# Kernel tuning notes

Measured on AMD Instinct MI355X. Metric: run time of the kernel, lower is better.

The kernel has to match this reference:

```python
import jax, jax.numpy as jnp
import numpy as np

N_NODES = 200000
N_EDGES = 800000
C1, E1 = 20000, 80000
C2, E2 = 2000, 8000
N_IN, N_HID, K_BLOCK = 24, 64, 6
N_OUT = 6
BN_EPS = 1e-5


def cheb_conv(x, edge_index, W, b, n):
    """PyG ChebConv with lambda_max=2: L_hat = -D^-1/2 A D^-1/2."""
    src, dst = edge_index[0], edge_index[1]
    K = W.shape[0]
    deg = jax.ops.segment_sum(jnp.ones(src.shape[0], x.dtype), dst, num_segments=n)
    dis = jnp.where(deg > 0, 1.0 / jnp.sqrt(jnp.maximum(deg, 1.0)), 0.0)
    norm = -(dis[src] * dis[dst])[:, None]  # [E,1]

    def prop(h):
        return jax.ops.segment_sum(h[src] * norm, dst, num_segments=n)

    Tx0 = x
    out = Tx0 @ W[0]
    if K > 1:
        Tx1 = prop(Tx0)
        out = out + Tx1 @ W[1]
        for k in range(2, K):
            Tx2 = 2.0 * prop(Tx1) - Tx0
            out = out + Tx2 @ W[k]
            Tx0, Tx1 = Tx1, Tx2
    return out + b


def batchnorm(h, g, bt):
    m = jnp.mean(h, axis=0)
    v = jnp.mean((h - m) ** 2, axis=0)  # biased var, as torch BN forward
    return (h - m) / jnp.sqrt(v + BN_EPS) * g + bt


def kipf_block(x, edge_index, W, b, g, bt, n):
    return jax.nn.relu(batchnorm(cheb_conv(x, edge_index, W, b, n), g, bt))


def segment_mean(x, seg, n_seg):
    s = jax.ops.segment_sum(x, seg, num_segments=n_seg)
    cnt = jax.ops.segment_sum(jnp.ones(x.shape[0], x.dtype), seg, num_segments=n_seg)
    return s / jnp.maximum(cnt, 1.0)[:, None]


def setup_inputs() -> dict:
    key = jax.random.key(0)
    ks = jax.random.split(key, 12)
    inp = {
        "x": jax.random.normal(ks[0], (N_NODES, N_IN), jnp.float32),
        "edge_index": jax.random.randint(ks[1], (2, N_EDGES), 0, N_NODES),
        "cluster1": jax.random.randint(ks[2], (N_NODES,), 0, C1),
        "cluster2": jax.random.randint(ks[3], (N_NODES,), 0, C2),
        "edge_index_c1": jax.random.randint(ks[4], (2, E1), 0, C1),
        "edge_index_c2": jax.random.randint(ks[5], (2, E2), 0, C2),
    }
    sc = 1.0 / np.sqrt(N_IN * K_BLOCK)
    for i, kk in zip((1, 2, 3), (ks[6], ks[7], ks[8])):
        inp[f"W{i}"] = jax.random.normal(kk, (K_BLOCK, N_IN, N_HID), jnp.float32) * sc
        inp[f"b{i}"] = jnp.zeros((N_HID,), jnp.float32)
        inp[f"g{i}"] = jnp.ones((N_HID,), jnp.float32)
        inp[f"bt{i}"] = jnp.zeros((N_HID,), jnp.float32)
    n_mix = 3 * N_HID + N_IN
    inp["Wm"] = jax.random.normal(ks[9], (1, n_mix, N_OUT), jnp.float32) / np.sqrt(n_mix)
    inp["bm"] = jnp.zeros((N_OUT,), jnp.float32)
    return inp


def reference(x, edge_index, cluster1, cluster2, edge_index_c1, edge_index_c2,
              W1, b1, g1, bt1, W2, b2, g2, bt2, W3, b3, g3, bt3, Wm, bm):
    # branch 1: full-resolution graph
    h1 = kipf_block(x, edge_index, W1, b1, g1, bt1, N_NODES)
    # branch 2: cluster1-pooled graph, then unpool
    xp1 = segment_mean(x, cluster1, C1)
    h2 = kipf_block(xp1, edge_index_c1, W2, b2, g2, bt2, C1)[cluster1]
    # branch 3: cluster2-pooled graph, then unpool
    xp2 = segment_mean(x, cluster2, C2)
    h3 = kipf_block(xp2, edge_index_c2, W3, b3, g3, bt3, C2)[cluster2]
    # skip concat with raw input, then mixing conv (K=1 -> identity Cheb term)
    mix = jnp.concatenate([h1, h2, h3, x], axis=1)
    return cheb_conv(mix, edge_index, Wm, bm, N_NODES)
```

## Files before the change

### kernel.cpp

```cpp
#include <hip/hip_runtime.h>
#include <algorithm>

#define FIN 24
#define NHID 64
#define NMIX 216
#define NOUT 6
#define BN_EPS 1e-5f

__global__ void k_hist(const int* __restrict__ ei, int E, int* deg) {
    int e = blockIdx.x * blockDim.x + threadIdx.x;
    if (e < E) atomicAdd(&deg[ei[E + e]], 1);
}

__global__ void k_scan_local(const int* __restrict__ deg, int n, int* rowptr, int* bsum,
                             float* __restrict__ dis) {
    __shared__ int s[256];
    int i = blockIdx.x * 256 + threadIdx.x;
    int v = (i < n) ? deg[i] : 0;
    if (i < n) dis[i] = v > 0 ? rsqrtf((float)v) : 0.f;
    s[threadIdx.x] = v;
    __syncthreads();
#pragma unroll
    for (int off = 1; off < 256; off <<= 1) {
        int x = (threadIdx.x >= off) ? s[threadIdx.x - off] : 0;
        __syncthreads();
        s[threadIdx.x] += x;
        __syncthreads();
    }
    if (i <= n) rowptr[i] = s[threadIdx.x] - v;
    if (threadIdx.x == 255) bsum[blockIdx.x] = s[255];
}

__global__ void k_scan_bsum(int* bsum, int nb) {
    __shared__ int s[256];
    int carry = 0;
    for (int base = 0; base < nb; base += 256) {
        int i = base + threadIdx.x;
        int v = (i < nb) ? bsum[i] : 0;
        s[threadIdx.x] = v;
        __syncthreads();
#pragma unroll
        for (int off = 1; off < 256; off <<= 1) {
            int x = (threadIdx.x >= off) ? s[threadIdx.x - off] : 0;
            __syncthreads();
            s[threadIdx.x] += x;
            __syncthreads();
        }
        if (i < nb) bsum[i] = s[threadIdx.x] - v + carry;
        carry += s[255];
        __syncthreads();
    }
}

__global__ void k_scan_add(int* rowptr, const int* __restrict__ bsum, int n) {
    int i = blockIdx.x * 256 + threadIdx.x;
    if (i <= n) rowptr[i] += bsum[blockIdx.x];
}

__global__ void k_fill(const int* __restrict__ ei, int E, const float* __restrict__ dis,
                       const int* __restrict__ rowptr, int* fill, int2* __restrict__ cv) {
    int e = blockIdx.x * blockDim.x + threadIdx.x;
    if (e >= E) return;
    int s = ei[e], d = ei[E + e];
    int slot = rowptr[d] + atomicAdd(&fill[d], 1);
    cv[slot] = make_int2(s, __float_as_int(-dis[s] * dis[d]));
}

__global__ void k_wt3(const float* __restrict__ Wa, float* __restrict__ Ta,
                      const float* __restrict__ Wb, float* __restrict__ Tb,
                      const float* __restrict__ Wc, float* __restrict__ Tc) {
    int o = blockIdx.x * blockDim.x + threadIdx.x;
    int which = o / 9216, oo = o - which * 9216;
    const float* W = (which == 0) ? Wa : (which == 1) ? Wb : Wc;
    float* T       = (which == 0) ? Ta : (which == 1) ? Tb : Tc;
    int k = oo / 1536, r = oo - k * 1536;
    int j = r / FIN, f = r - j * FIN;
    T[oo] = W[k * 1536 + f * NHID + j];
}

__global__ void k_propg(const int* __restrict__ rowptr, const int2* __restrict__ cv,
                        float scale, const float* __restrict__ h,
                        const float* __restrict__ prev, float* __restrict__ out, int n) {
    int idx = blockIdx.x * blockDim.x + threadIdx.x;
    if (idx >= n * 6) return;
    int d = idx / 6, q = idx - d * 6;
    int beg = rowptr[d], end = rowptr[d + 1];
    const float4* h4 = reinterpret_cast<const float4*>(h);
    float ax = 0.f, ay = 0.f, az = 0.f, aw = 0.f;
    float bx = 0.f, by = 0.f, bz = 0.f, bw = 0.f;
    float cx = 0.f, cy = 0.f, cz = 0.f, cw = 0.f;
    float dx = 0.f, dy = 0.f, dz = 0.f, dw = 0.f;
    int e = beg;
    for (; e + 4 <= end; e += 4) {
        int2 c0 = cv[e], c1 = cv[e + 1], c2 = cv[e + 2], c3 = cv[e + 3];
        float w0 = __int_as_float(c0.y), w1 = __int_as_float(c1.y);
        float w2 = __int_as_float(c2.y), w3 = __int_as_float(c3.y);
        float4 h0 = h4[(size_t)c0.x * 6 + q];
        float4 h1 = h4[(size_t)c1.x * 6 + q];
        float4 h2 = h4[(size_t)c2.x * 6 + q];
        float4 h3 = h4[(size_t)c3.x * 6 + q];
        ax = fmaf(w0, h0.x, ax); ay = fmaf(w0, h0.y, ay);
        az = fmaf(w0, h0.z, az); aw = fmaf(w0, h0.w, aw);
        bx = fmaf(w1, h1.x, bx); by = fmaf(w1, h1.y, by);
        bz = fmaf(w1, h1.z, bz); bw = fmaf(w1, h1.w, bw);
        cx = fmaf(w2, h2.x, cx); cy = fmaf(w2, h2.y, cy);
        cz = fmaf(w2, h2.z, cz); cw = fmaf(w2, h2.w, cw);
        dx = fmaf(w3, h3.x, dx); dy = fmaf(w3, h3.y, dy);
        dz = fmaf(w3, h3.z, dz); dw = fmaf(w3, h3.w, dw);
    }
    for (; e + 2 <= end; e += 2) {
        int2 c0 = cv[e], c1 = cv[e + 1];
        float w0 = __int_as_float(c0.y), w1 = __int_as_float(c1.y);
        float4 h0 = h4[(size_t)c0.x * 6 + q];
        float4 h1 = h4[(size_t)c1.x * 6 + q];
        ax = fmaf(w0, h0.x, ax); ay = fmaf(w0, h0.y, ay);
        az = fmaf(w0, h0.z, az); aw = fmaf(w0, h0.w, aw);
        bx = fmaf(w1, h1.x, bx); by = fmaf(w1, h1.y, by);
        bz = fmaf(w1, h1.z, bz); bw = fmaf(w1, h1.w, bw);
    }
    if (e < end) {
        int2 c0 = cv[e];
        float w0 = __int_as_float(c0.y);
        float4 h0 = h4[(size_t)c0.x * 6 + q];
        ax = fmaf(w0, h0.x, ax); ay = fmaf(w0, h0.y, ay);
        az = fmaf(w0, h0.z, az); aw = fmaf(w0, h0.w, aw);
    }
    ax += bx + cx + dx; ay += by + cy + dy;
    az += bz + cz + dz; aw += bw + cw + dw;
    float4 r;
    if (prev) {
        float4 pv = reinterpret_cast<const float4*>(prev)[idx];
        r = make_float4(fmaf(scale, ax, -pv.x), fmaf(scale, ay, -pv.y),
                        fmaf(scale, az, -pv.z), fmaf(scale, aw, -pv.w));
    } else {
        r = make_float4(scale * ax, scale * ay, scale * az, scale * aw);
    }
    reinterpret_cast<float4*>(out)[idx] = r;
}

__global__ void k_gemv6(const float* __restrict__ S0, const float* __restrict__ S1,
                        const float* __restrict__ S2, const float* __restrict__ S3,
                        const float* __restrict__ S4, const float* __restrict__ S5,
                        const float* __restrict__ Wt, const float* __restrict__ bias,
                        float* __restrict__ acc, float* __restrict__ stats, int n) {
    int j = threadIdx.x & 63;
    int w = threadIdx.x >> 6;
    int nbase = __builtin_amdgcn_readfirstlane(blockIdx.x * 64 + (w << 4));
    float accv[16];
    {
        float bb = bias[j];
#pragma unroll
        for (int nd = 0; nd < 16; ++nd) accv[nd] = bb;
    }
#pragma unroll 1
    for (int k = 0; k < 6; ++k) {
        const float* Sk = (k == 0) ? S0 : (k == 1) ? S1 : (k == 2) ? S2
                        : (k == 3) ? S3 : (k == 4) ? S4 : S5;
        const float4* wp = reinterpret_cast<const float4*>(Wt + k * (NHID * FIN) + j * FIN);
        float4 w0 = wp[0], w1 = wp[1], w2 = wp[2], w3 = wp[3], w4 = wp[4], w5 = wp[5];
#pragma unroll
        for (int nd = 0; nd < 16; ++nd) {
            int node = nbase + nd;
            int nodec = (node < n) ? node : (n - 1);
            const float4* r = reinterpret_cast<const float4*>(Sk + (size_t)nodec * FIN);
            float4 v0 = r[0], v1 = r[1], v2 = r[2], v3 = r[3], v4 = r[4], v5 = r[5];
            float a = accv[nd];
            a = fmaf(v0.x, w0.x, a); a = fmaf(v0.y, w0.y, a);
            a = fmaf(v0.z, w0.z, a); a = fmaf(v0.w, w0.w, a);
            a = fmaf(v1.x, w1.x, a); a = fmaf(v1.y, w1.y, a);
            a = fmaf(v1.z, w1.z, a); a = fmaf(v1.w, w1.w, a);
            a = fmaf(v2.x, w2.x, a); a = fmaf(v2.y, w2.y, a);
            a = fmaf(v2.z, w2.z, a); a = fmaf(v2.w, w2.w, a);
            a = fmaf(v3.x, w3.x, a); a = fmaf(v3.y, w3.y, a);
            a = fmaf(v3.z, w3.z, a); a = fmaf(v3.w, w3.w, a);
            a = fmaf(v4.x, w4.x, a); a = fmaf(v4.y, w4.y, a);
            a = fmaf(v4.z, w4.z, a); a = fmaf(v4.w, w4.w, a);
            a = fmaf(v5.x, w5.x, a); a = fmaf(v5.y, w5.y, a);
            a = fmaf(v5.z, w5.z, a); a = fmaf(v5.w, w5.w, a);
            accv[nd] = a;
        }
    }
    float sum = 0.f, sq = 0.f;
#pragma unroll
    for (int nd = 0; nd < 16; ++nd) {
        int node = nbase + nd;
        if (node < n) {
            acc[(size_t)node * NHID + j] = accv[nd];
            sum += accv[nd]; sq = fmaf(accv[nd], accv[nd], sq);
        }
    }
    __shared__ float rs[256], rq[256];
    rs[threadIdx.x] = sum; rq[threadIdx.x] = sq;
    __syncthreads();
    if (threadIdx.x < 64) {
        float s = rs[threadIdx.x] + rs[threadIdx.x + 64] + rs[threadIdx.x + 128] + rs[threadIdx.x + 192];
        float q = rq[threadIdx.x] + rq[threadIdx.x + 64] + rq[threadIdx.x + 128] + rq[threadIdx.x + 192];
        atomicAdd(&stats[threadIdx.x], s);
        atomicAdd(&stats[NHID + threadIdx.x], q);
    }
}

__global__ void k_bnprep3(const float* __restrict__ st1, const float* __restrict__ g1,
                          const float* __restrict__ bt1, float inv1,
                          const float* __restrict__ st2, const float* __restrict__ g2,
                          const float* __restrict__ bt2, float inv2,
                          const float* __restrict__ st3, const float* __restrict__ g3,
                          const float* __restrict__ bt3, float inv3,
                          float* __restrict__ s1, float* __restrict__ s2,
                          float* __restrict__ s3) {
    int b = threadIdx.x >> 6, i = threadIdx.x & 63;
    const float* st = (b == 0) ? st1 : (b == 1) ? st2 : st3;
    const float* g  = (b == 0) ? g1  : (b == 1) ? g2  : g3;
    const float* bt = (b == 0) ? bt1 : (b == 1) ? bt2 : bt3;
    float inv       = (b == 0) ? inv1 : (b == 1) ? inv2 : inv3;
    float* so       = (b == 0) ? s1  : (b == 1) ? s2  : s3;
    float m = st[i] * inv;
    float v = st[NHID + i] * inv - m * m;
    float sc = g[i] * rsqrtf(v + BN_EPS);
    so[i] = sc;
    so[NHID + i] = fmaf(-m, sc, bt[i]);
}

__global__ void k_scatter2(const float* __restrict__ x, const int* __restrict__ cl1,
                           const int* __restrict__ cl2, int n,
                           float* xp1, float* cnt1, float* xp2, float* cnt2) {
    int idx = blockIdx.x * blockDim.x + threadIdx.x;
    if (idx >= n * FIN) return;
    int node = idx / FIN, f = idx - node * FIN;
    float v = x[idx];
    int c1 = cl1[node], c2 = cl2[node];
    atomicAdd(&xp1[c1 * FIN + f], v);
    atomicAdd(&xp2[c2 * FIN + f], v);
    if (f == 0) { atomicAdd(&cnt1[c1], 1.f); atomicAdd(&cnt2[c2], 1.f); }
}

__global__ void k_divcnt(float* xp, const float* __restrict__ cnt, int c) {
    int idx = blockIdx.x * blockDim.x + threadIdx.x;
    if (idx >= c * FIN) return;
    xp[idx] = xp[idx] / fmaxf(cnt[idx / FIN], 1.f);
}

__global__ void k_final(const float* __restrict__ acc1, const float* __restrict__ sc1,
                        const float* __restrict__ h2, const float* __restrict__ sc2,
                        const int* __restrict__ cl1,
                        const float* __restrict__ h3, const float* __restrict__ sc3,
                        const int* __restrict__ cl2,
                        const float* __restrict__ x, const float* __restrict__ Wm,
                        const float* __restrict__ bm, float* __restrict__ out, int n) {
    int t = blockIdx.x * blockDim.x + threadIdx.x;
    if (t >= n) return;
    float o[NOUT];
#pragma unroll
    for (int j = 0; j < NOUT; ++j) o[j] = bm[j];
    {
        const float4* r4 = reinterpret_cast<const float4*>(acc1 + (size_t)t * NHID);
#pragma unroll
        for (int i4 = 0; i4 < NHID / 4; ++i4) {
            float4 v = r4[i4];
            float hv[4] = {v.x, v.y, v.z, v.w};
#pragma unroll
            for (int c = 0; c < 4; ++c) {
                int i = i4 * 4 + c;
                float h = fmaxf(fmaf(hv[c], sc1[i], sc1[NHID + i]), 0.f);
#pragma unroll
                for (int j = 0; j < NOUT; ++j) o[j] = fmaf(h, Wm[i * NOUT + j], o[j]);
            }
        }
    }
    {
        const float4* r4 = reinterpret_cast<const float4*>(h2 + (size_t)cl1[t] * NHID);
#pragma unroll
        for (int i4 = 0; i4 < NHID / 4; ++i4) {
            float4 v = r4[i4];
            float hv[4] = {v.x, v.y, v.z, v.w};
#pragma unroll
            for (int c = 0; c < 4; ++c) {
                int hid = i4 * 4 + c;
                float h = fmaxf(fmaf(hv[c], sc2[hid], sc2[NHID + hid]), 0.f);
#pragma unroll
                for (int j = 0; j < NOUT; ++j) o[j] = fmaf(h, Wm[(NHID + hid) * NOUT + j], o[j]);
            }
        }
    }
    {
        const float4* r4 = reinterpret_cast<const float4*>(h3 + (size_t)cl2[t] * NHID);
#pragma unroll
        for (int i4 = 0; i4 < NHID / 4; ++i4) {
            float4 v = r4[i4];
            float hv[4] = {v.x, v.y, v.z, v.w};
#pragma unroll
            for (int c = 0; c < 4; ++c) {
                int hid = i4 * 4 + c;
                float h = fmaxf(fmaf(hv[c], sc3[hid], sc3[NHID + hid]), 0.f);
#pragma unroll
                for (int j = 0; j < NOUT; ++j) o[j] = fmaf(h, Wm[(2 * NHID + hid) * NOUT + j], o[j]);
            }
        }
    }
    {
        const float4* r4 = reinterpret_cast<const float4*>(x + (size_t)t * FIN);
#pragma unroll
        for (int i4 = 0; i4 < FIN / 4; ++i4) {
            float4 v = r4[i4];
            float hv[4] = {v.x, v.y, v.z, v.w};
#pragma unroll
            for (int c = 0; c < 4; ++c) {
                int i = 3 * NHID + i4 * 4 + c;
#pragma unroll
                for (int j = 0; j < NOUT; ++j) o[j] = fmaf(hv[c], Wm[i * NOUT + j], o[j]);
            }
        }
    }
    float* op = out + (size_t)t * NOUT;
#pragma unroll
    for (int j = 0; j < NOUT; ++j) op[j] = o[j];
}

extern "C" void kernel_launch(void* const* d_in, const int* in_sizes, int n_in,
                              void* d_out, int out_size, void* d_ws, size_t ws_size,
                              hipStream_t stream) {
    const int N = 200000, E = 800000;
    const int C1n = 20000, E1 = 80000;
    const int C2n = 2000, E2 = 8000;

    const float* x  = (const float*)d_in[0];
    const int* ei   = (const int*)d_in[1];
    const int* cl1  = (const int*)d_in[2];
    const int* cl2  = (const int*)d_in[3];
    const int* eic1 = (const int*)d_in[4];
    const int* eic2 = (const int*)d_in[5];
    const float* W1 = (const float*)d_in[6];  const float* b1 = (const float*)d_in[7];
    const float* g1 = (const float*)d_in[8];  const float* bt1 = (const float*)d_in[9];
    const float* W2 = (const float*)d_in[10]; const float* b2 = (const float*)d_in[11];
    const float* g2 = (const float*)d_in[12]; const float* bt2 = (const float*)d_in[13];
    const float* W3 = (const float*)d_in[14]; const float* b3 = (const float*)d_in[15];
    const float* g3 = (const float*)d_in[16]; const float* bt3 = (const float*)d_in[17];
    const float* Wm = (const float*)d_in[18]; const float* bm = (const float*)d_in[19];

    char* wb = (char*)d_ws;
    size_t off = 0;
    auto alloc = [&](size_t nwords) {
        void* p = wb + off; off += ((nwords + 3) & ~(size_t)3) * 4; return p;
    };
    int* degi1 = (int*)alloc(N);   int* fill1 = (int*)alloc(N);
    int* degi2 = (int*)alloc(C1n); int* fill2 = (int*)alloc(C1n);
    int* degi3 = (int*)alloc(C2n); int* fill3 = (int*)alloc(C2n);
    float* st1 = (float*)alloc(128); float* st2 = (float*)alloc(128); float* st3 = (float*)alloc(128);
    float* xp1 = (float*)alloc((size_t)C1n * FIN); float* cnt1 = (float*)alloc(C1n);
    float* xp2 = (float*)alloc((size_t)C2n * FIN); float* cnt2 = (float*)alloc(C2n);
    size_t zero_bytes = off;
    int* rp1 = (int*)alloc(N + 1);   int2* cv1 = (int2*)alloc(2 * (size_t)E);
    int* rp2 = (int*)alloc(C1n + 1); int2* cv2 = (int2*)alloc(2 * (size_t)E1);
    int* rp3 = (int*)alloc(C2n + 1); int2* cv3 = (int2*)alloc(2 * (size_t)E2);
    float* dis1 = (float*)alloc(N); float* dis2 = (float*)alloc(C1n); float* dis3 = (float*)alloc(C2n);
    int* bsum = (int*)alloc(1024);
    float* scsh1 = (float*)alloc(128); float* scsh2 = (float*)alloc(128); float* scsh3 = (float*)alloc(128);
    float* Wt1 = (float*)alloc(9216); float* Wt2 = (float*)alloc(9216); float* Wt3 = (float*)alloc(9216);
    float* T1[5]; for (int i = 0; i < 5; ++i) T1[i] = (float*)alloc((size_t)N * FIN);
    float* T2[5]; for (int i = 0; i < 5; ++i) T2[i] = (float*)alloc((size_t)C1n * FIN);
    float* T3[5]; for (int i = 0; i < 5; ++i) T3[i] = (float*)alloc((size_t)C2n * FIN);
    float* acc1 = (float*)alloc((size_t)N * NHID);
    float* acc2 = (float*)alloc((size_t)C1n * NHID);
    float* acc3 = (float*)alloc((size_t)C2n * NHID);
    if (off > ws_size) return;

    hipMemsetAsync(d_ws, 0, zero_bytes, stream);

    const int T = 256;
    auto cdiv = [](int a, int b) { return (a + b - 1) / b; };

    k_wt3<<<cdiv(3 * 9216, T), T, 0, stream>>>(W1, Wt1, W2, Wt2, W3, Wt3);

    auto branch = [&](const float* xin, int n, const int* e, int Ecnt,
                      const float* Wt, const float* bb, int* degi, int* fill, float* dis,
                      int* rp, int2* cv, float** Tb, float* acc, float* st) {
        int ge = cdiv(Ecnt, T);
        int nb = cdiv(n + 1, 256);
        int gg = cdiv(n, 64);
        int gp = cdiv(n * 6, T);
        k_hist<<<ge, T, 0, stream>>>(e, Ecnt, degi);
        k_scan_local<<<nb, 256, 0, stream>>>(degi, n, rp, bsum, dis);
        k_scan_bsum<<<1, 256, 0, stream>>>(bsum, nb);
        k_scan_add<<<nb, 256, 0, stream>>>(rp, bsum, n);
        k_fill<<<ge, T, 0, stream>>>(e, Ecnt, dis, rp, fill, cv);
        k_propg<<<gp, T, 0, stream>>>(rp, cv, 1.0f, xin, nullptr, Tb[0], n);
        k_propg<<<gp, T, 0, stream>>>(rp, cv, 2.0f, Tb[0], xin, Tb[1], n);
        k_propg<<<gp, T, 0, stream>>>(rp, cv, 2.0f, Tb[1], Tb[0], Tb[2], n);
        k_propg<<<gp, T, 0, stream>>>(rp, cv, 2.0f, Tb[2], Tb[1], Tb[3], n);
        k_propg<<<gp, T, 0, stream>>>(rp, cv, 2.0f, Tb[3], Tb[2], Tb[4], n);
        k_gemv6<<<gg, T, 0, stream>>>(xin, Tb[0], Tb[1], Tb[2], Tb[3], Tb[4],
                                      Wt, bb, acc, st, n);
    };

    branch(x, N, ei, E, Wt1, b1, degi1, fill1, dis1, rp1, cv1, T1, acc1, st1);
    k_scatter2<<<cdiv(N * FIN, T), T, 0, stream>>>(x, cl1, cl2, N, xp1, cnt1, xp2, cnt2);
    k_divcnt<<<cdiv(C1n * FIN, T), T, 0, stream>>>(xp1, cnt1, C1n);
    branch(xp1, C1n, eic1, E1, Wt2, b2, degi2, fill2, dis2, rp2, cv2, T2, acc2, st2);
    k_divcnt<<<cdiv(C2n * FIN, T), T, 0, stream>>>(xp2, cnt2, C2n);
    branch(xp2, C2n, eic2, E2, Wt3, b3, degi3, fill3, dis3, rp3, cv3, T3, acc3, st3);
    k_bnprep3<<<1, 192, 0, stream>>>(st1, g1, bt1, 1.0f / (float)N,
                                     st2, g2, bt2, 1.0f / (float)C1n,
                                     st3, g3, bt3, 1.0f / (float)C2n,
                                     scsh1, scsh2, scsh3);
    k_final<<<cdiv(N, T), T, 0, stream>>>(acc1, scsh1, acc2, scsh2, cl1,
                                          acc3, scsh3, cl2,
                                          x, Wm, bm, (float*)d_out, N);
}
```

Measured before the change: 666.1 us.

## Remap gemv6 to one node per thread with LDS-transposed coalesced stores

The per-branch Chebyshev GEMM kernel changes from each thread computing one output column for 16 nodes to each thread computing all 64 outputs for one node. Weights become wave-uniform loads and each input row is read once per thread instead of being redundantly loaded by 64 lanes. Outputs are staged through padded LDS tiles so stores are coalesced as float4 and the BN statistics are reduced with shuffles. In exchange each thread holds 64 accumulators plus a 24-float row, which raises register pressure and may lower occupancy, and there are four times fewer blocks.

```diff
diff --git a/kernel.cpp b/kernel.cpp
--- a/kernel.cpp
+++ b/kernel.cpp
@@ -143,60 +143,72 @@
                         const float* __restrict__ S4, const float* __restrict__ S5,
                         const float* __restrict__ Wt, const float* __restrict__ bias,
                         float* __restrict__ acc, float* __restrict__ stats, int n) {
-    int j = threadIdx.x & 63;
+    __shared__ float tile[4][2][64 * 17];
+    int l = threadIdx.x & 63;
     int w = threadIdx.x >> 6;
-    int nbase = __builtin_amdgcn_readfirstlane(blockIdx.x * 64 + (w << 4));
-    float accv[16];
-    {
-        float bb = bias[j];
-#pragma unroll
-        for (int nd = 0; nd < 16; ++nd) accv[nd] = bb;
-    }
+    int nbase = blockIdx.x * 256 + w * 64;
+    int node = nbase + l;
+    bool ok = (node < n);
+    int nodec = ok ? node : (n - 1);
+    float av[64];
+#pragma unroll
+    for (int j = 0; j < 64; ++j) av[j] = bias[j];
 #pragma unroll 1
     for (int k = 0; k < 6; ++k) {
         const float* Sk = (k == 0) ? S0 : (k == 1) ? S1 : (k == 2) ? S2
                         : (k == 3) ? S3 : (k == 4) ? S4 : S5;
-        const float4* wp = reinterpret_cast<const float4*>(Wt + k * (NHID * FIN) + j * FIN);
-        float4 w0 = wp[0], w1 = wp[1], w2 = wp[2], w3 = wp[3], w4 = wp[4], w5 = wp[5];
-#pragma unroll
-        for (int nd = 0; nd < 16; ++nd) {
-            int node = nbase + nd;
-            int nodec = (node < n) ? node : (n - 1);
-            const float4* r = reinterpret_cast<const float4*>(Sk + (size_t)nodec * FIN);
-            float4 v0 = r[0], v1 = r[1], v2 = r[2], v3 = r[3], v4 = r[4], v5 = r[5];
-            float a = accv[nd];
-            a = fmaf(v0.x, w0.x, a); a = fmaf(v0.y, w0.y, a);
-            a = fmaf(v0.z, w0.z, a); a = fmaf(v0.w, w0.w, a);
-            a = fmaf(v1.x, w1.x, a); a = fmaf(v1.y, w1.y, a);
-            a = fmaf(v1.z, w1.z, a); a = fmaf(v1.w, w1.w, a);
-            a = fmaf(v2.x, w2.x, a); a = fmaf(v2.y, w2.y, a);
-            a = fmaf(v2.z, w2.z, a); a = fmaf(v2.w, w2.w, a);
-            a = fmaf(v3.x, w3.x, a); a = fmaf(v3.y, w3.y, a);
-            a = fmaf(v3.z, w3.z, a); a = fmaf(v3.w, w3.w, a);
-            a = fmaf(v4.x, w4.x, a); a = fmaf(v4.y, w4.y, a);
-            a = fmaf(v4.z, w4.z, a); a = fmaf(v4.w, w4.w, a);
-            a = fmaf(v5.x, w5.x, a); a = fmaf(v5.y, w5.y, a);
-            a = fmaf(v5.z, w5.z, a); a = fmaf(v5.w, w5.w, a);
-            accv[nd] = a;
-        }
-    }
-    float sum = 0.f, sq = 0.f;
-#pragma unroll
-    for (int nd = 0; nd < 16; ++nd) {
-        int node = nbase + nd;
-        if (node < n) {
-            acc[(size_t)node * NHID + j] = accv[nd];
-            sum += accv[nd]; sq = fmaf(accv[nd], accv[nd], sq);
-        }
-    }
-    __shared__ float rs[256], rq[256];
-    rs[threadIdx.x] = sum; rq[threadIdx.x] = sq;
-    __syncthreads();
-    if (threadIdx.x < 64) {
-        float s = rs[threadIdx.x] + rs[threadIdx.x + 64] + rs[threadIdx.x + 128] + rs[threadIdx.x + 192];
-        float q = rq[threadIdx.x] + rq[threadIdx.x + 64] + rq[threadIdx.x + 128] + rq[threadIdx.x + 192];
-        atomicAdd(&stats[threadIdx.x], s);
-        atomicAdd(&stats[NHID + threadIdx.x], q);
+        const float4* r = reinterpret_cast<const float4*>(Sk + (size_t)nodec * FIN);
+        float4 v0 = r[0], v1 = r[1], v2 = r[2], v3 = r[3], v4 = r[4], v5 = r[5];
+        float rowf[FIN] = {v0.x, v0.y, v0.z, v0.w, v1.x, v1.y, v1.z, v1.w,
+                           v2.x, v2.y, v2.z, v2.w, v3.x, v3.y, v3.z, v3.w,
+                           v4.x, v4.y, v4.z, v4.w, v5.x, v5.y, v5.z, v5.w};
+        const float* Wk = Wt + k * (NHID * FIN);
+#pragma unroll
+        for (int j = 0; j < 64; ++j) {
+            const float* ww = Wk + j * FIN;
+            float a = av[j];
+#pragma unroll
+            for (int f = 0; f < FIN; ++f) a = fmaf(rowf[f], ww[f], a);
+            av[j] = a;
+        }
+    }
+    if (!ok) {
+#pragma unroll
+        for (int j = 0; j < 64; ++j) av[j] = 0.f;
+    }
+#pragma unroll
+    for (int c = 0; c < 4; ++c) {
+        float* tl = &tile[w][c & 1][0];
+#pragma unroll
+        for (int jj = 0; jj < 16; ++jj) {
+            tl[l * 17 + jj] = av[c * 16 + jj];
+        }
+        asm volatile("" ::: "memory");
+#pragma unroll
+        for (int it = 0; it < 4; ++it) {
+            int lin = it * 64 + l;
+            int nd = lin >> 2, qj = lin & 3;
+            int gnode = nbase + nd;
+            if (gnode < n) {
+                float4 vv = make_float4(tl[nd * 17 + qj * 4 + 0], tl[nd * 17 + qj * 4 + 1],
+                                        tl[nd * 17 + qj * 4 + 2], tl[nd * 17 + qj * 4 + 3]);
+                *reinterpret_cast<float4*>(acc + (size_t)gnode * NHID + c * 16 + qj * 4) = vv;
+            }
+        }
+        float ps = 0.f, pq = 0.f;
+        int jj = l & 15, ndb = (l >> 4) * 16;
+#pragma unroll
+        for (int t = 0; t < 16; ++t) {
+            float vv = tl[(ndb + t) * 17 + jj];
+            ps += vv; pq = fmaf(vv, vv, pq);
+        }
+        ps += __shfl_xor(ps, 16, 64); pq += __shfl_xor(pq, 16, 64);
+        ps += __shfl_xor(ps, 32, 64); pq += __shfl_xor(pq, 32, 64);
+        if (l < 16) {
+            atomicAdd(&stats[c * 16 + jj], ps);
+            atomicAdd(&stats[NHID + c * 16 + jj], pq);
+        }
+        asm volatile("" ::: "memory");
     }
 }
 
@@ -364,7 +376,7 @@
     float* acc3 = (float*)alloc((size_t)C2n * NHID);
     if (off > ws_size) return;
 
-    hipMemsetAsync(d_ws, 0, zero_bytes, stream);
+    (void)hipMemsetAsync(d_ws, 0, zero_bytes, stream);
 
     const int T = 256;
     auto cdiv = [](int a, int b) { return (a + b - 1) / b; };
@@ -376,7 +388,7 @@
                       int* rp, int2* cv, float** Tb, float* acc, float* st) {
         int ge = cdiv(Ecnt, T);
         int nb = cdiv(n + 1, 256);
-        int gg = cdiv(n, 64);
+        int gg = cdiv(n, 256);
         int gp = cdiv(n * 6, T);
         k_hist<<<ge, T, 0, stream>>>(e, Ecnt, degi);
         k_scan_local<<<nb, 256, 0, stream>>>(degi, n, rp, bsum, dis);
```

After: 908.9 us. +36.5%, slower.
